# Kernel optimization log

Hardware: AMD Instinct MI355X
Metric: run time of the kernel (lower is better)

The kernel has to match this reference:

```python
import jax, jax.numpy as jnp
import numpy as np

B, S, DM, H = 2, 2048, 1024, 16        # dim_model = d_model//2 = 1024
WINDOW, DILATION, N_GLOBAL = 513, 2, 32
HD = DM // H
NEG = -1e9


def build_mask(n, window_size, dilation, global_idx):
    # dilated local window: |i-j| <= (window//2)*dilation and (i-j) % dilation == 0
    i = jnp.arange(n)[:, None]
    j = jnp.arange(n)[None, :]
    d = j - i
    half = window_size // 2
    local = (jnp.abs(d) <= half * dilation) & (jnp.mod(d, dilation) == 0)
    g = jnp.zeros((n,), bool).at[global_idx].set(True)
    # symmetric global token mask: global rows and columns fully attend
    return local | g[:, None] | g[None, :]


def setup_inputs() -> dict:
    key = jax.random.key(0)
    ks = jax.random.split(key, 9)
    std = 0.02
    inp = {
        "q": jax.random.normal(ks[0], (B, S, DM), jnp.float32),
        "k": jax.random.normal(ks[1], (B, S, DM), jnp.float32),
        "v": jax.random.normal(ks[2], (B, S, DM), jnp.float32),
        "Wq": jax.random.normal(ks[3], (DM, DM), jnp.float32) * std,
        "Wk": jax.random.normal(ks[4], (DM, DM), jnp.float32) * std,
        "Wv": jax.random.normal(ks[5], (DM, DM), jnp.float32) * std,
        "Wo": jax.random.normal(ks[6], (DM, DM), jnp.float32) * std,
        "bq": jnp.zeros((DM,), jnp.float32),
        "bk": jnp.zeros((DM,), jnp.float32),
        "bv": jnp.zeros((DM,), jnp.float32),
        "bo": jnp.zeros((DM,), jnp.float32),
        "global_idx": jax.random.randint(ks[7], (N_GLOBAL,), 0, S, jnp.int64)
        if jax.config.jax_enable_x64 else jax.random.randint(ks[7], (N_GLOBAL,), 0, S, jnp.int32),
    }
    return inp


def reference(q, k, v, Wq, Wk, Wv, Wo, bq, bk, bv, bo, global_idx):
    def split(x):  # [B,S,DM] -> [B,H,S,HD]
        return x.reshape(B, S, H, HD).transpose(0, 2, 1, 3)

    qh = split(q @ Wq.T + bq)
    kh = split(k @ Wk.T + bk)
    vh = split(v @ Wv.T + bv)

    scores = jnp.einsum("bhqd,bhkd->bhqk", qh, kh) / jnp.sqrt(jnp.asarray(HD, qh.dtype))
    mask = build_mask(S, WINDOW, DILATION, global_idx)  # [S,S] bool
    scores = jnp.where(mask[None, None], scores, NEG)
    attn = jax.nn.softmax(scores, axis=-1)
    out = jnp.einsum("bhqk,bhkd->bhqd", attn, vh)
    out = out.transpose(0, 2, 1, 3).reshape(B, S, DM)
    return out @ Wo.T + bo
```

## Files before the change

### kernel.cpp

```cpp
#include <hip/hip_runtime.h>
#include <hip/hip_bf16.h>
#include <math.h>

#define BB 2
#define SS 2048
#define DMM 1024
#define HH 16
#define HDD 64
#define NGLOB 32
#define MM 4096

typedef __attribute__((ext_vector_type(8))) short short8;
typedef __attribute__((ext_vector_type(4))) float float4v;

__device__ __forceinline__ short f2bf(float f) {
    union { float f; unsigned u; } x; x.f = f;
    unsigned r = (x.u + 0x7fffu + ((x.u >> 16) & 1u)) >> 16;
    return (short)r;
}

#define ASYNC16(gp, lp) __builtin_amdgcn_global_load_lds( \
    (__attribute__((address_space(1))) void*)(gp), \
    (__attribute__((address_space(3))) void*)(lp), 16, 0, 0)

__global__ void setup_globals(const int* __restrict__ gidx, int* __restrict__ g,
                              int* __restrict__ glist, int* __restrict__ gcount) {
    int t = threadIdx.x;
    for (int i = t; i < SS; i += 256) g[i] = 0;
    if (t == 0) *gcount = 0;
    __syncthreads();
    if (t < NGLOB) {
        int j = gidx[t];
        if (j >= 0 && j < SS) g[j] = 1;
    }
    __syncthreads();
    for (int j = t; j < SS; j += 256) {
        if (g[j]) {
            int p = atomicAdd(gcount, 1);
            glist[p] = j;
        }
    }
}

__global__ __launch_bounds__(256)
void convert_all(const float* __restrict__ q, const float* __restrict__ k,
                 const float* __restrict__ v,
                 const float* __restrict__ w0, const float* __restrict__ w1,
                 const float* __restrict__ w2, const float* __restrict__ w3,
                 short* __restrict__ abf, short* __restrict__ wbf) {
    int z = blockIdx.y;
    const float* src;
    short* dst;
    size_t n;
    if (z < 3) {
        src = (z == 0) ? q : (z == 1) ? k : v;
        dst = abf + (size_t)z * ((size_t)MM * DMM);
        n = (size_t)MM * DMM;
    } else {
        int y = z - 3;
        src = (y == 0) ? w0 : (y == 1) ? w1 : (y == 2) ? w2 : w3;
        dst = wbf + (size_t)y * ((size_t)DMM * DMM);
        n = (size_t)DMM * DMM;
    }
    size_t i = ((size_t)blockIdx.x * 256 + threadIdx.x) * 8;
    if (i >= n) return;
    float4 a = *(const float4*)(src + i);
    float4 b = *(const float4*)(src + i + 4);
    short8 s;
    s[0]=f2bf(a.x); s[1]=f2bf(a.y); s[2]=f2bf(a.z); s[3]=f2bf(a.w);
    s[4]=f2bf(b.x); s[5]=f2bf(b.y); s[6]=f2bf(b.z); s[7]=f2bf(b.w);
    *(short8*)(dst + i) = s;
}

template<int OBF, int HEADSPLIT>
__global__ __launch_bounds__(256)
void gemm64(const short* __restrict__ Abase, const short* __restrict__ Wbase,
            const float* __restrict__ b0, const float* __restrict__ b1,
            const float* __restrict__ b2,
            void* __restrict__ O0p, void* __restrict__ O1p, void* __restrict__ O2p) {
    __shared__ short As[64 * 32];
    __shared__ short Ws[128 * 32];

    int t = threadIdx.x;
    int z = blockIdx.y;
    const short* A    = Abase + (size_t)z * ((size_t)MM * DMM);
    const short* W    = Wbase + (size_t)z * ((size_t)DMM * DMM);
    const float* bias = (z == 0) ? b0 : (z == 1) ? b1 : b2;
    void* outp        = (z == 0) ? O0p : (z == 1) ? O1p : O2p;

    int bid = blockIdx.x;
    int xcd = bid & 7, loc = bid >> 3;
    int nblk = loc & 7, mloc = loc >> 3;
    int m0 = (xcd * 8 + mloc) * 64;
    int n0 = nblk * 128;

    int lane = t & 63, w = t >> 6;
    int quad = lane >> 4, col = lane & 15;
    int arow0 = (w & 1) * 32;
    int ncol0 = (w >> 1) * 64;

    float4v acc[2][4];
    #pragma unroll
    for (int i = 0; i < 2; i++)
        #pragma unroll
        for (int j = 0; j < 4; j++) acc[i][j] = (float4v){0, 0, 0, 0};

    int rowA = t >> 2,  kcA = (t & 3) * 8;

    for (int it = 0; it < 32; it++) {
        int k0 = it * 32;
        ASYNC16(A + (size_t)(m0 + rowA) * DMM + k0 + kcA,      &As[t * 8]);
        ASYNC16(W + (size_t)(n0 + rowA) * DMM + k0 + kcA,      &Ws[t * 8]);
        ASYNC16(W + (size_t)(n0 + 64 + rowA) * DMM + k0 + kcA, &Ws[2048 + t * 8]);
        __syncthreads();

        short8 aF[2], bF[4];
        #pragma unroll
        for (int i = 0; i < 2; i++)
            aF[i] = *(short8*)&As[(arow0 + 16 * i + col) * 32 + quad * 8];
        #pragma unroll
        for (int j = 0; j < 4; j++)
            bF[j] = *(short8*)&Ws[(ncol0 + 16 * j + col) * 32 + quad * 8];

        #pragma unroll
        for (int i = 0; i < 2; i++)
            #pragma unroll
            for (int j = 0; j < 4; j++)
                acc[i][j] = __builtin_amdgcn_mfma_f32_16x16x32_bf16(aF[i], bF[j], acc[i][j], 0, 0, 0);
        __syncthreads();
    }

    #pragma unroll
    for (int i = 0; i < 2; i++) {
        #pragma unroll
        for (int j = 0; j < 4; j++) {
            int n = n0 + ncol0 + 16 * j + col;
            float bn = bias[n];
            #pragma unroll
            for (int r = 0; r < 4; r++) {
                int m = m0 + arow0 + 16 * i + quad * 4 + r;
                float val = acc[i][j][r] + bn;
                size_t idx;
                if (HEADSPLIT) {
                    int b = m >> 11;
                    int s = m & 2047;
                    int h = n >> 6;
                    int hd = n & 63;
                    idx = (((size_t)b * HH + h) * SS + s) * HDD + hd;
                } else {
                    idx = (size_t)m * DMM + n;
                }
                if (OBF) ((short*)outp)[idx] = f2bf(val);
                else     ((float*)outp)[idx] = val;
            }
        }
    }
}

__global__ __launch_bounds__(256)
void band_attn(const short* __restrict__ qh, const short* __restrict__ kh,
               const short* __restrict__ vh, const int* __restrict__ glist,
               const int* __restrict__ gcount, short* __restrict__ ao) {
    __shared__ short Qs[64 * 72];
    __shared__ short Ks[32 * 72];
    __shared__ short Vt[64 * 40];
    __shared__ short Ps[4 * 16 * 40];
    __shared__ int   gjs[32];

    int t = threadIdx.x;
    int qt = blockIdx.x, h = blockIdx.y, z = blockIdx.z;
    int b = z >> 1, p = z & 1;
    int qq0 = qt * 64;
    int nG = *gcount;

    const short* Qb = qh + ((size_t)(b * HH + h) * SS) * HDD;
    const short* Kb = kh + ((size_t)(b * HH + h) * SS) * HDD;
    const short* Vb = vh + ((size_t)(b * HH + h) * SS) * HDD;

    int row8 = t >> 3;
    int dim8 = (t & 7) * 8;

    #pragma unroll
    for (int rr = 0; rr < 2; rr++) {
        int row = rr * 32 + row8;
        int i = 2 * (qq0 + row) + p;
        short8 qv = *(const short8*)(Qb + (size_t)i * HDD + dim8);
        *(short8*)&Qs[row * 72 + dim8] = qv;
    }
    if (t < 32) gjs[t] = (t < nG) ? glist[t] : -1000000;
    __syncthreads();

    int lane = t & 63, w = t >> 6;
    int quad = lane >> 4, col = lane & 15;

    short8 qf0 = *(short8*)&Qs[(16 * w + col) * 72 + quad * 8];
    short8 qf1 = *(short8*)&Qs[(16 * w + col) * 72 + 32 + quad * 8];

    float4v O0 = {0,0,0,0}, O1 = {0,0,0,0}, O2 = {0,0,0,0}, O3 = {0,0,0,0};
    float lst[4] = {0.f, 0.f, 0.f, 0.f};

    for (int c = 0; c < 19; c++) {
        __syncthreads();
        int ch0 = qq0 - 256 + c * 32;
        int srow;
        if (c < 18) srow = 2 * (ch0 + row8) + p;
        else        srow = (row8 < nG) ? gjs[row8] : 0;
        srow = srow < 0 ? 0 : (srow > SS - 1 ? SS - 1 : srow);
        short8 kv = *(const short8*)(Kb + (size_t)srow * HDD + dim8);
        short8 vv = *(const short8*)(Vb + (size_t)srow * HDD + dim8);
        *(short8*)&Ks[row8 * 72 + dim8] = kv;
        #pragma unroll
        for (int j = 0; j < 8; j++) Vt[(dim8 + j) * 40 + row8] = vv[j];
        __syncthreads();

        short8 kA0 = *(short8*)&Ks[col * 72 + quad * 8];
        short8 kA1 = *(short8*)&Ks[col * 72 + 32 + quad * 8];
        short8 kB0 = *(short8*)&Ks[(16 + col) * 72 + quad * 8];
        short8 kB1 = *(short8*)&Ks[(16 + col) * 72 + 32 + quad * 8];
        float4v sA = {0,0,0,0}, sB = {0,0,0,0};
        sA = __builtin_amdgcn_mfma_f32_16x16x32_bf16(qf0, kA0, sA, 0, 0, 0);
        sA = __builtin_amdgcn_mfma_f32_16x16x32_bf16(qf1, kA1, sA, 0, 0, 0);
        sB = __builtin_amdgcn_mfma_f32_16x16x32_bf16(qf0, kB0, sB, 0, 0, 0);
        sB = __builtin_amdgcn_mfma_f32_16x16x32_bf16(qf1, kB1, sB, 0, 0, 0);

        #pragma unroll
        for (int r = 0; r < 4; r++) {
            int q  = 16 * w + quad * 4 + r;
            int qq = qq0 + q;
            bool vA, vB;
            if (c < 18) {
                int jA = ch0 + col, jB = jA + 16;
                int dA = jA - qq; dA = dA < 0 ? -dA : dA;
                int dB = jB - qq; dB = dB < 0 ? -dB : dB;
                vA = (jA >= 0) && (jA < 1024) && (dA <= 256);
                vB = (jB >= 0) && (jB < 1024) && (dB <= 256);
            } else {
                int i = 2 * qq + p;
                int jA = gjs[col], jB = gjs[col + 16];
                int dA = jA - i, dB = jB - i;
                int aA = dA < 0 ? -dA : dA;
                int aB = dB < 0 ? -dB : dB;
                vA = (jA >= 0) && !((aA <= 512) && ((dA & 1) == 0));
                vB = (jB >= 0) && !((aB <= 512) && ((dB & 1) == 0));
            }
            float pa = vA ? __expf(sA[r] * 0.125f) : 0.f;
            float pb = vB ? __expf(sB[r] * 0.125f) : 0.f;
            lst[r] += pa + pb;
            Ps[(w * 16 + quad * 4 + r) * 40 + col]      = f2bf(pa);
            Ps[(w * 16 + quad * 4 + r) * 40 + col + 16] = f2bf(pb);
        }
        asm volatile("s_waitcnt lgkmcnt(0)" ::: "memory");

        short8 pf  = *(short8*)&Ps[(w * 16 + col) * 40 + quad * 8];
        short8 vf0 = *(short8*)&Vt[(col) * 40 + quad * 8];
        short8 vf1 = *(short8*)&Vt[(16 + col) * 40 + quad * 8];
        short8 vf2 = *(short8*)&Vt[(32 + col) * 40 + quad * 8];
        short8 vf3 = *(short8*)&Vt[(48 + col) * 40 + quad * 8];
        O0 = __builtin_amdgcn_mfma_f32_16x16x32_bf16(pf, vf0, O0, 0, 0, 0);
        O1 = __builtin_amdgcn_mfma_f32_16x16x32_bf16(pf, vf1, O1, 0, 0, 0);
        O2 = __builtin_amdgcn_mfma_f32_16x16x32_bf16(pf, vf2, O2, 0, 0, 0);
        O3 = __builtin_amdgcn_mfma_f32_16x16x32_bf16(pf, vf3, O3, 0, 0, 0);
    }

    #pragma unroll
    for (int r = 0; r < 4; r++) {
        float l = lst[r];
        #pragma unroll
        for (int mk = 1; mk < 16; mk <<= 1) l += __shfl_xor(l, mk);
        float inv = 1.0f / l;
        int q = 16 * w + quad * 4 + r;
        int i = 2 * (qq0 + q) + p;
        short* dst = ao + ((size_t)b * SS + i) * DMM + h * HDD;
        dst[col]      = f2bf(O0[r] * inv);
        dst[col + 16] = f2bf(O1[r] * inv);
        dst[col + 32] = f2bf(O2[r] * inv);
        dst[col + 48] = f2bf(O3[r] * inv);
    }
}

__global__ __launch_bounds__(256)
void global_part(const short* __restrict__ qh, const short* __restrict__ kh,
                 const short* __restrict__ vh, const int* __restrict__ glist,
                 const int* __restrict__ gcount,
                 float* __restrict__ pl, float* __restrict__ pO) {
    __shared__ short Qs[32 * 72];
    __shared__ short Ks[2][32 * 72];
    __shared__ short Vt[2][64 * 40];
    __shared__ short Ps[4 * 16 * 40];

    int t = threadIdx.x;
    int s = blockIdx.x, h = blockIdx.y, b = blockIdx.z;
    int nG = *gcount;

    const short* Qb = qh + ((size_t)(b * HH + h) * SS) * HDD;
    const short* Kb = kh + ((size_t)(b * HH + h) * SS) * HDD;
    const short* Vb = vh + ((size_t)(b * HH + h) * SS) * HDD;

    int row8 = t >> 3, dim8 = (t & 7) * 8;
    {
        int cq = row8 < nG ? row8 : 0;
        int src = glist[cq];
        short8 qv = *(const short8*)(Qb + (size_t)src * HDD + dim8);
        *(short8*)&Qs[row8 * 72 + dim8] = qv;
    }
    __syncthreads();

    int lane = t & 63, w = t >> 6;
    int quad = lane >> 4, col = lane & 15;
    int g = w >> 1, qt = w & 1;

    short8 qf0 = *(short8*)&Qs[(qt * 16 + col) * 72 + quad * 8];
    short8 qf1 = *(short8*)&Qs[(qt * 16 + col) * 72 + 32 + quad * 8];

    float4v O0 = {0,0,0,0}, O1 = {0,0,0,0}, O2 = {0,0,0,0}, O3 = {0,0,0,0};
    float lst[4] = {0.f, 0.f, 0.f, 0.f};

    int js0 = s * 256;
    for (int it = 0; it < 4; it++) {
        __syncthreads();
        int r64 = t >> 2, dimb = (t & 3) * 16;
        int j = js0 + it * 64 + r64;
        const short* kp = Kb + (size_t)j * HDD + dimb;
        const short* vp = Vb + (size_t)j * HDD + dimb;
        short8 k0 = *(const short8*)kp, k1 = *(const short8*)(kp + 8);
        short8 v0 = *(const short8*)vp, v1 = *(const short8*)(vp + 8);
        int half = r64 >> 5, r32 = r64 & 31;
        *(short8*)&Ks[half][r32 * 72 + dimb]     = k0;
        *(short8*)&Ks[half][r32 * 72 + dimb + 8] = k1;
        #pragma unroll
        for (int u = 0; u < 8; u++) Vt[half][(dimb + u) * 40 + r32]     = v0[u];
        #pragma unroll
        for (int u = 0; u < 8; u++) Vt[half][(dimb + 8 + u) * 40 + r32] = v1[u];
        __syncthreads();

        short8 kA0 = *(short8*)&Ks[g][col * 72 + quad * 8];
        short8 kA1 = *(short8*)&Ks[g][col * 72 + 32 + quad * 8];
        short8 kB0 = *(short8*)&Ks[g][(16 + col) * 72 + quad * 8];
        short8 kB1 = *(short8*)&Ks[g][(16 + col) * 72 + 32 + quad * 8];
        float4v sA = {0,0,0,0}, sB = {0,0,0,0};
        sA = __builtin_amdgcn_mfma_f32_16x16x32_bf16(qf0, kA0, sA, 0, 0, 0);
        sA = __builtin_amdgcn_mfma_f32_16x16x32_bf16(qf1, kA1, sA, 0, 0, 0);
        sB = __builtin_amdgcn_mfma_f32_16x16x32_bf16(qf0, kB0, sB, 0, 0, 0);
        sB = __builtin_amdgcn_mfma_f32_16x16x32_bf16(qf1, kB1, sB, 0, 0, 0);

        #pragma unroll
        for (int r = 0; r < 4; r++) {
            float pa = __expf(sA[r] * 0.125f);
            float pb = __expf(sB[r] * 0.125f);
            lst[r] += pa + pb;
            Ps[(w * 16 + quad * 4 + r) * 40 + col]      = f2bf(pa);
            Ps[(w * 16 + quad * 4 + r) * 40 + col + 16] = f2bf(pb);
        }
        asm volatile("s_waitcnt lgkmcnt(0)" ::: "memory");

        short8 pf  = *(short8*)&Ps[(w * 16 + col) * 40 + quad * 8];
        short8 vf0 = *(short8*)&Vt[g][(col) * 40 + quad * 8];
        short8 vf1 = *(short8*)&Vt[g][(16 + col) * 40 + quad * 8];
        short8 vf2 = *(short8*)&Vt[g][(32 + col) * 40 + quad * 8];
        short8 vf3 = *(short8*)&Vt[g][(48 + col) * 40 + quad * 8];
        O0 = __builtin_amdgcn_mfma_f32_16x16x32_bf16(pf, vf0, O0, 0, 0, 0);
        O1 = __builtin_amdgcn_mfma_f32_16x16x32_bf16(pf, vf1, O1, 0, 0, 0);
        O2 = __builtin_amdgcn_mfma_f32_16x16x32_bf16(pf, vf2, O2, 0, 0, 0);
        O3 = __builtin_amdgcn_mfma_f32_16x16x32_bf16(pf, vf3, O3, 0, 0, 0);
    }

    int sp = s * 2 + g;
    size_t base = ((size_t)(b * HH + h) * 16 + sp) * 32;
    #pragma unroll
    for (int r = 0; r < 4; r++) {
        float l = lst[r];
        #pragma unroll
        for (int mk = 1; mk < 16; mk <<= 1) l += __shfl_xor(l, mk);
        int q = qt * 16 + quad * 4 + r;
        if (col == 0) pl[base + q] = l;
        float* Od = pO + (base + q) * 64;
        Od[col]      = O0[r];
        Od[col + 16] = O1[r];
        Od[col + 32] = O2[r];
        Od[col + 48] = O3[r];
    }
}

__global__ __launch_bounds__(256)
void global_merge(const float* __restrict__ pl, const float* __restrict__ pO,
                  const int* __restrict__ glist, const int* __restrict__ gcount,
                  short* __restrict__ ao) {
    int h = blockIdx.x, b = blockIdx.y;
    int t = threadIdx.x;
    int d = t & 63, qg = t >> 6;
    int nG = *gcount;
    size_t bh = ((size_t)(b * HH + h) * 16) * 32;

    for (int q = qg; q < nG; q += 4) {
        float L = 0.f, acc = 0.f;
        #pragma unroll
        for (int sp = 0; sp < 16; sp++) {
            L   += pl[bh + sp * 32 + q];
            acc += pO[(bh + sp * 32 + q) * 64 + d];
        }
        int i = glist[q];
        ao[((size_t)b * SS + i) * DMM + h * HDD + d] = f2bf(acc / L);
    }
}

extern "C" void kernel_launch(void* const* d_in, const int* in_sizes, int n_in,
                              void* d_out, int out_size, void* d_ws, size_t ws_size,
                              hipStream_t stream) {
    const float* q  = (const float*)d_in[0];
    const float* k  = (const float*)d_in[1];
    const float* v  = (const float*)d_in[2];
    const float* Wq = (const float*)d_in[3];
    const float* Wk = (const float*)d_in[4];
    const float* Wv = (const float*)d_in[5];
    const float* Wo = (const float*)d_in[6];
    const float* bq = (const float*)d_in[7];
    const float* bk = (const float*)d_in[8];
    const float* bv = (const float*)d_in[9];
    const float* bo = (const float*)d_in[10];
    const int* gidx = (const int*)d_in[11];
    float* out = (float*)d_out;

    const size_t NE = (size_t)BB * SS * DMM;
    const size_t WE = (size_t)DMM * DMM;
    int*   g      = (int*)d_ws;
    int*   glist  = g + SS;
    int*   gcount = glist + SS;
    short* qh     = (short*)((char*)d_ws + 32768);
    short* kh     = qh + NE;
    short* vh     = kh + NE;
    short* ao     = vh + NE;
    short* wbf    = ao + NE;
    short* wo     = wbf + 3 * WE;
    short* abf    = wbf + 4 * WE;
    float* pl     = (float*)abf;
    float* pO     = pl + 16384;

    setup_globals<<<1, 256, 0, stream>>>(gidx, g, glist, gcount);

    dim3 gc(2048, 7);
    convert_all<<<gc, 256, 0, stream>>>(q, k, v, Wq, Wk, Wv, Wo, abf, wbf);

    dim3 gq(512, 3);
    gemm64<1, 1><<<gq, 256, 0, stream>>>(abf, wbf, bq, bk, bv, qh, kh, vh);

    dim3 ga(16, HH, BB * 2);
    band_attn<<<ga, 256, 0, stream>>>(qh, kh, vh, glist, gcount, ao);

    dim3 gp(8, HH, BB);
    global_part<<<gp, 256, 0, stream>>>(qh, kh, vh, glist, gcount, pl, pO);

    dim3 gm(HH, BB);
    global_merge<<<gm, 256, 0, stream>>>(pl, pO, glist, gcount, ao);

    dim3 go(512, 1);
    gemm64<0, 0><<<go, 256, 0, stream>>>(ao, wo, bo, bo, bo, out, out, out);
}
```

Measured before the change: 244.3 us.

## Swizzle transposed V in LDS, remap attention blocks per XCD, use exp2

Stores the transposed V tile in shared memory with an XOR swizzle on the key index, in both the band and global-part kernels, to reduce LDS bank conflicts on the scattered transposed writes. The band attention grid becomes 1D, with block IDs remapped so that each XCD handles a contiguous group of (batch, parity, head) slices, aiming for better L2 reuse of K/V. Softmax exponentials switch from __expf with a 0.125 scale to exp2f with a pre-multiplied log2e scale. The band mask test is simplified to a precomputed lo/hi column range per row. The new index arithmetic adds ALU work, and the remap assumes the hardware dispatches blocks round-robin across eight XCDs.

```diff
diff --git a/kernel.cpp b/kernel.cpp
--- a/kernel.cpp
+++ b/kernel.cpp
@@ -9,6 +9,7 @@
 #define HDD 64
 #define NGLOB 32
 #define MM 4096
+#define SCALE2 0.18033688f
 
 typedef __attribute__((ext_vector_type(8))) short short8;
 typedef __attribute__((ext_vector_type(4))) float float4v;
@@ -22,6 +23,8 @@
 #define ASYNC16(gp, lp) __builtin_amdgcn_global_load_lds( \
     (__attribute__((address_space(1))) void*)(gp), \
     (__attribute__((address_space(3))) void*)(lp), 16, 0, 0)
+
+#define VSL(dim, key) ((dim) * 40 + (((((key) >> 3) ^ (((dim) >> 3) & 3)) << 3) | ((key) & 7)))
 
 __global__ void setup_globals(const int* __restrict__ gidx, int* __restrict__ g,
                               int* __restrict__ glist, int* __restrict__ gcount) {
@@ -168,7 +171,13 @@
     __shared__ int   gjs[32];
 
     int t = threadIdx.x;
-    int qt = blockIdx.x, h = blockIdx.y, z = blockIdx.z;
+    int bid = blockIdx.x;
+    int xcd = bid & 7, idx = bid >> 3;
+    int gl  = idx >> 4;
+    int qt  = idx & 15;
+    int gid = xcd * 8 + gl;
+    int z   = gid >> 4;
+    int h   = gid & 15;
     int b = z >> 1, p = z & 1;
     int qq0 = qt * 64;
     int nG = *gcount;
@@ -210,7 +219,10 @@
         short8 vv = *(const short8*)(Vb + (size_t)srow * HDD + dim8);
         *(short8*)&Ks[row8 * 72 + dim8] = kv;
         #pragma unroll
-        for (int j = 0; j < 8; j++) Vt[(dim8 + j) * 40 + row8] = vv[j];
+        for (int j = 0; j < 8; j++) {
+            int d = dim8 + j;
+            Vt[VSL(d, row8)] = vv[j];
+        }
         __syncthreads();
 
         short8 kA0 = *(short8*)&Ks[col * 72 + quad * 8];
@@ -223,39 +235,48 @@
         sB = __builtin_amdgcn_mfma_f32_16x16x32_bf16(qf0, kB0, sB, 0, 0, 0);
         sB = __builtin_amdgcn_mfma_f32_16x16x32_bf16(qf1, kB1, sB, 0, 0, 0);
 
-        #pragma unroll
-        for (int r = 0; r < 4; r++) {
-            int q  = 16 * w + quad * 4 + r;
-            int qq = qq0 + q;
-            bool vA, vB;
-            if (c < 18) {
-                int jA = ch0 + col, jB = jA + 16;
-                int dA = jA - qq; dA = dA < 0 ? -dA : dA;
-                int dB = jB - qq; dB = dB < 0 ? -dB : dB;
-                vA = (jA >= 0) && (jA < 1024) && (dA <= 256);
-                vB = (jB >= 0) && (jB < 1024) && (dB <= 256);
-            } else {
+        if (c < 18) {
+            int nlo = -ch0;
+            int nhi = 1023 - ch0;
+            #pragma unroll
+            for (int r = 0; r < 4; r++) {
+                int qq = qq0 + 16 * w + quad * 4 + r;
+                int u  = qq - ch0;
+                int lo = max(u - 256, nlo);
+                int hi = min(u + 256, nhi);
+                bool vA = (col >= lo) && (col <= hi);
+                bool vB = (col + 16 >= lo) && (col + 16 <= hi);
+                float pa = vA ? exp2f(sA[r] * SCALE2) : 0.f;
+                float pb = vB ? exp2f(sB[r] * SCALE2) : 0.f;
+                lst[r] += pa + pb;
+                Ps[(w * 16 + quad * 4 + r) * 40 + col]      = f2bf(pa);
+                Ps[(w * 16 + quad * 4 + r) * 40 + col + 16] = f2bf(pb);
+            }
+        } else {
+            #pragma unroll
+            for (int r = 0; r < 4; r++) {
+                int qq = qq0 + 16 * w + quad * 4 + r;
                 int i = 2 * qq + p;
                 int jA = gjs[col], jB = gjs[col + 16];
                 int dA = jA - i, dB = jB - i;
                 int aA = dA < 0 ? -dA : dA;
                 int aB = dB < 0 ? -dB : dB;
-                vA = (jA >= 0) && !((aA <= 512) && ((dA & 1) == 0));
-                vB = (jB >= 0) && !((aB <= 512) && ((dB & 1) == 0));
+                bool vA = (jA >= 0) && !((aA <= 512) && ((dA & 1) == 0));
+                bool vB = (jB >= 0) && !((aB <= 512) && ((dB & 1) == 0));
+                float pa = vA ? exp2f(sA[r] * SCALE2) : 0.f;
+                float pb = vB ? exp2f(sB[r] * SCALE2) : 0.f;
+                lst[r] += pa + pb;
+                Ps[(w * 16 + quad * 4 + r) * 40 + col]      = f2bf(pa);
+                Ps[(w * 16 + quad * 4 + r) * 40 + col + 16] = f2bf(pb);
             }
-            float pa = vA ? __expf(sA[r] * 0.125f) : 0.f;
-            float pb = vB ? __expf(sB[r] * 0.125f) : 0.f;
-            lst[r] += pa + pb;
-            Ps[(w * 16 + quad * 4 + r) * 40 + col]      = f2bf(pa);
-            Ps[(w * 16 + quad * 4 + r) * 40 + col + 16] = f2bf(pb);
         }
         asm volatile("s_waitcnt lgkmcnt(0)" ::: "memory");
 
         short8 pf  = *(short8*)&Ps[(w * 16 + col) * 40 + quad * 8];
-        short8 vf0 = *(short8*)&Vt[(col) * 40 + quad * 8];
-        short8 vf1 = *(short8*)&Vt[(16 + col) * 40 + quad * 8];
-        short8 vf2 = *(short8*)&Vt[(32 + col) * 40 + quad * 8];
-        short8 vf3 = *(short8*)&Vt[(48 + col) * 40 + quad * 8];
+        short8 vf0 = *(short8*)&Vt[(col) * 40 + ((quad ^ ((col >> 3) & 3)) << 3)];
+        short8 vf1 = *(short8*)&Vt[(16 + col) * 40 + ((quad ^ (((16 + col) >> 3) & 3)) << 3)];
+        short8 vf2 = *(short8*)&Vt[(32 + col) * 40 + ((quad ^ (((32 + col) >> 3) & 3)) << 3)];
+        short8 vf3 = *(short8*)&Vt[(48 + col) * 40 + ((quad ^ (((48 + col) >> 3) & 3)) << 3)];
         O0 = __builtin_amdgcn_mfma_f32_16x16x32_bf16(pf, vf0, O0, 0, 0, 0);
         O1 = __builtin_amdgcn_mfma_f32_16x16x32_bf16(pf, vf1, O1, 0, 0, 0);
         O2 = __builtin_amdgcn_mfma_f32_16x16x32_bf16(pf, vf2, O2, 0, 0, 0);
@@ -328,9 +349,15 @@
         *(short8*)&Ks[half][r32 * 72 + dimb]     = k0;
         *(short8*)&Ks[half][r32 * 72 + dimb + 8] = k1;
         #pragma unroll
-        for (int u = 0; u < 8; u++) Vt[half][(dimb + u) * 40 + r32]     = v0[u];
-        #pragma unroll
-        for (int u = 0; u < 8; u++) Vt[half][(dimb + 8 + u) * 40 + r32] = v1[u];
+        for (int u = 0; u < 8; u++) {
+            int d = dimb + u;
+            Vt[half][VSL(d, r32)] = v0[u];
+        }
+        #pragma unroll
+        for (int u = 0; u < 8; u++) {
+            int d = dimb + 8 + u;
+            Vt[half][VSL(d, r32)] = v1[u];
+        }
         __syncthreads();
 
         short8 kA0 = *(short8*)&Ks[g][col * 72 + quad * 8];
@@ -345,8 +372,8 @@
 
         #pragma unroll
         for (int r = 0; r < 4; r++) {
-            float pa = __expf(sA[r] * 0.125f);
-            float pb = __expf(sB[r] * 0.125f);
+            float pa = exp2f(sA[r] * SCALE2);
+            float pb = exp2f(sB[r] * SCALE2);
             lst[r] += pa + pb;
             Ps[(w * 16 + quad * 4 + r) * 40 + col]      = f2bf(pa);
             Ps[(w * 16 + quad * 4 + r) * 40 + col + 16] = f2bf(pb);
@@ -354,10 +381,10 @@
         asm volatile("s_waitcnt lgkmcnt(0)" ::: "memory");
 
         short8 pf  = *(short8*)&Ps[(w * 16 + col) * 40 + quad * 8];
-        short8 vf0 = *(short8*)&Vt[g][(col) * 40 + quad * 8];
-        short8 vf1 = *(short8*)&Vt[g][(16 + col) * 40 + quad * 8];
-        short8 vf2 = *(short8*)&Vt[g][(32 + col) * 40 + quad * 8];
-        short8 vf3 = *(short8*)&Vt[g][(48 + col) * 40 + quad * 8];
+        short8 vf0 = *(short8*)&Vt[g][(col) * 40 + ((quad ^ ((col >> 3) & 3)) << 3)];
+        short8 vf1 = *(short8*)&Vt[g][(16 + col) * 40 + ((quad ^ (((16 + col) >> 3) & 3)) << 3)];
+        short8 vf2 = *(short8*)&Vt[g][(32 + col) * 40 + ((quad ^ (((32 + col) >> 3) & 3)) << 3)];
+        short8 vf3 = *(short8*)&Vt[g][(48 + col) * 40 + ((quad ^ (((48 + col) >> 3) & 3)) << 3)];
         O0 = __builtin_amdgcn_mfma_f32_16x16x32_bf16(pf, vf0, O0, 0, 0, 0);
         O1 = __builtin_amdgcn_mfma_f32_16x16x32_bf16(pf, vf1, O1, 0, 0, 0);
         O2 = __builtin_amdgcn_mfma_f32_16x16x32_bf16(pf, vf2, O2, 0, 0, 0);
@@ -443,8 +470,7 @@
     dim3 gq(512, 3);
     gemm64<1, 1><<<gq, 256, 0, stream>>>(abf, wbf, bq, bk, bv, qh, kh, vh);
 
-    dim3 ga(16, HH, BB * 2);
-    band_attn<<<ga, 256, 0, stream>>>(qh, kh, vh, glist, gcount, ao);
+    band_attn<<<1024, 256, 0, stream>>>(qh, kh, vh, glist, gcount, ao);
 
     dim3 gp(8, HH, BB);
     global_part<<<gp, 256, 0, stream>>>(qh, kh, vh, glist, gcount, pl, pO);
```

After: 231.6 us. -5.2%, faster.
